# Optimization experiments

Measured on AMD Instinct MI355X. Metric: run time of the kernel, lower is better.

The kernel has to match this reference:

```python
import jax, jax.numpy as jnp
import numpy as np

NUM_HEADS = 12
HEAD_DIM = 64
HIDDEN = NUM_HEADS * HEAD_DIM


def setup_inputs() -> dict:
    key = jax.random.key(0)
    ks = jax.random.split(key, 10)
    B, S, N_ROT = 8, 1374, 1369
    s = 0.02
    return {
        "hidden_states": jax.random.normal(ks[0], (B, S, HIDDEN), jnp.float32),
        "sin": jax.random.normal(ks[1], (N_ROT, HEAD_DIM), jnp.float32),
        "cos": jax.random.normal(ks[2], (N_ROT, HEAD_DIM), jnp.float32),
        "Wq": jax.random.normal(ks[3], (HIDDEN, HIDDEN), jnp.float32) * s,
        "bq": jax.random.normal(ks[4], (HIDDEN,), jnp.float32) * s,
        "Wk": jax.random.normal(ks[5], (HIDDEN, HIDDEN), jnp.float32) * s,
        "Wv": jax.random.normal(ks[6], (HIDDEN, HIDDEN), jnp.float32) * s,
        "bv": jax.random.normal(ks[7], (HIDDEN,), jnp.float32) * s,
        "Wp": jax.random.normal(ks[8], (HIDDEN, HIDDEN), jnp.float32) * s,
        "bp": jax.random.normal(ks[9], (HIDDEN,), jnp.float32) * s,
    }


def _rotate_half(x):
    x1, x2 = jnp.split(x, 2, axis=-1)
    return jnp.concatenate([-x2, x1], axis=-1)


def _rope_apply(x, sin, cos):
    return x * cos + _rotate_half(x) * sin


def reference(hidden_states, sin, cos, Wq, bq, Wk, Wv, bv, Wp, bp):
    B, S, _ = hidden_states.shape
    scaling = HEAD_DIM ** -0.5

    def to_heads(x):  # [B,S,HIDDEN] -> [B,H,S,D]
        return x.reshape(B, S, NUM_HEADS, HEAD_DIM).transpose(0, 2, 1, 3)

    q = to_heads(hidden_states @ Wq.T + bq)
    k = to_heads(hidden_states @ Wk.T)  # no key bias (mask_k_bias)
    v = to_heads(hidden_states @ Wv.T + bv)

    # RoPE only on patch tokens (prefix = cls + register tokens untouched)
    prefix = S - sin.shape[-2]
    q = jnp.concatenate([q[:, :, :prefix], _rope_apply(q[:, :, prefix:], sin, cos)], axis=2)
    k = jnp.concatenate([k[:, :, :prefix], _rope_apply(k[:, :, prefix:], sin, cos)], axis=2)

    # eager attention: softmax in float32, no mask, no dropout (eval)
    scores = jnp.einsum("bhqd,bhkd->bhqk", q, k) * scaling
    probs = jax.nn.softmax(scores.astype(jnp.float32), axis=-1).astype(q.dtype)
    ctx = jnp.einsum("bhqk,bhkd->bqhd", probs, v).reshape(B, S, HIDDEN)
    return ctx @ Wp.T + bp
```

## Files before the change

kernel.cpp:

```cpp
#include <hip/hip_runtime.h>
#include <stdint.h>

typedef unsigned short u16;
typedef unsigned int u32;
typedef u16 u16x8 __attribute__((ext_vector_type(8)));
typedef __bf16 bf16x8 __attribute__((ext_vector_type(8)));
typedef float f32x4 __attribute__((ext_vector_type(4)));

#define S_LEN 1374
#define S_PAD 1408
#define PRE_TOK 5
#define HID 768
#define NH 12
#define MPAD 11008

__device__ __forceinline__ u16 f2bf(float f) {
    union { float f; u32 u; } v; v.f = f;
    u32 r = v.u + 0x7fffu + ((v.u >> 16) & 1u);
    return (u16)(r >> 16);
}
__device__ __forceinline__ bf16x8 as_bf(u16x8 v) { bf16x8 r; __builtin_memcpy(&r, &v, 16); return r; }
__device__ __forceinline__ bf16x8 lds_load8(const u16* p) {
    u16x8 t = *(const u16x8*)p;
    return as_bf(t);
}
__device__ __forceinline__ u32 cvtpk_bf16(float lo, float hi) {
    u32 r;
    asm("v_cvt_pk_bf16_f32 %0, %1, %2" : "=v"(r) : "v"(lo), "v"(hi));
    return r;
}
__device__ __forceinline__ float fexp2(float x) {
    float r;
    asm("v_exp_f32 %0, %1" : "=v"(r) : "v"(x));
    return r;
}
__device__ __forceinline__ void gload16(void* lds, const void* g) {
    unsigned int __attribute__((address_space(1)))* gp =
        (unsigned int __attribute__((address_space(1)))*)(unsigned long long)g;
    unsigned int __attribute__((address_space(3)))* lp =
        (unsigned int __attribute__((address_space(3)))*)(unsigned int)(unsigned long long)lds;
    __builtin_amdgcn_global_load_lds(gp, lp, 16, 0, 0);
}


__global__ __launch_bounds__(256) void pack_x(const float* __restrict__ X, u16* __restrict__ Xb) {
    size_t i = (size_t)blockIdx.x * 256 + threadIdx.x;
    size_t e = i * 8;
    const size_t TOT = (size_t)10992 * HID;
    u16x8 o = {0,0,0,0,0,0,0,0};
    if (e < TOT) {
        f32x4 a = *(const f32x4*)(X + e);
        f32x4 b = *(const f32x4*)(X + e + 4);
#pragma unroll
        for (int j = 0; j < 4; ++j) { o[j] = f2bf(a[j]); o[4 + j] = f2bf(b[j]); }
    }
    *(u16x8*)(Xb + e) = o;
}

__global__ __launch_bounds__(256) void pack_w(
    const float* __restrict__ Wq, const float* __restrict__ Wk, const float* __restrict__ Wv,
    const float* __restrict__ Wp, const float* __restrict__ bq, const float* __restrict__ bv,
    u16* __restrict__ wqkv, u16* __restrict__ wpb, float* __restrict__ bqkv)
{
    int g = blockIdx.x * 256 + threadIdx.x;
    const int QKV8 = 2304 * HID / 8;
    const int P8 = HID * HID / 8;
    if (g < QKV8) {
        int e = g * 8;
        int row = e / HID, col = e - row * HID;
        const float* src = (row < 768) ? (Wq + (size_t)row * HID + col)
                         : (row < 1536) ? (Wk + (size_t)(row - 768) * HID + col)
                                        : (Wv + (size_t)(row - 1536) * HID + col);
        u16x8 o;
#pragma unroll
        for (int j = 0; j < 8; ++j) o[j] = f2bf(src[j]);
        *(u16x8*)(wqkv + e) = o;
    } else if (g < QKV8 + P8) {
        int e = (g - QKV8) * 8;
        u16x8 o;
#pragma unroll
        for (int j = 0; j < 8; ++j) o[j] = f2bf(Wp[e + j]);
        *(u16x8*)(wpb + e) = o;
    }
    if (g < 288) {
        int e = g * 8;
#pragma unroll
        for (int j = 0; j < 8; ++j) {
            int c = e + j;
            bqkv[c] = (c < 768) ? bq[c] : (c < 1536 ? 0.f : bv[c - 1536]);
        }
    }
}


template <int EPI>
__global__ __launch_bounds__(256) void gemm_nt(
    const u16* __restrict__ A, const u16* __restrict__ B, const float* __restrict__ bias,
    float* __restrict__ Yf, u16* __restrict__ Qh, u16* __restrict__ Kh,
    u16* __restrict__ Yv, const float* __restrict__ SN, const float* __restrict__ CS,
    int N, int K)
{
    __shared__ u16 As[128 * 64];
    __shared__ u16 Bs[128 * 64];
    int tid = threadIdx.x;
    int w = tid >> 6, l = tid & 63;
    int fr = l & 15, fg = l >> 4;
    int row0 = blockIdx.y * 128;
    int col0 = blockIdx.x * 128;
    int wr = (w >> 1) * 64, wc = (w & 1) * 64;

    f32x4 zero4 = {0.f, 0.f, 0.f, 0.f};
    f32x4 acc[4][4];
#pragma unroll
    for (int m = 0; m < 4; ++m)
#pragma unroll
        for (int n = 0; n < 4; ++n) acc[m][n] = zero4;

    int srow[4], soff[4];
#pragma unroll
    for (int i = 0; i < 4; ++i) {
        int sbyte = (i * 4 + w) * 1024 + l * 16;
        int r = sbyte >> 7;
        int ir = (sbyte & 127) ^ ((r & 7) << 4);
        srow[i] = r; soff[i] = ir >> 1;
    }

    for (int kt = 0; kt < K; kt += 64) {
#pragma unroll
        for (int i = 0; i < 4; ++i) {
            int sb = (i * 4 + w) * 1024;
            gload16((char*)As + sb, A + (size_t)(row0 + srow[i]) * K + kt + soff[i]);
            gload16((char*)Bs + sb, B + (size_t)(col0 + srow[i]) * K + kt + soff[i]);
        }
        __syncthreads();
#pragma unroll
        for (int c = 0; c < 2; ++c) {
            bf16x8 af[4], bfr[4];
#pragma unroll
            for (int m = 0; m < 4; ++m) {
                int r = wr + m * 16 + fr;
                int byte_ = (c * 64 + fg * 16) ^ ((r & 7) << 4);
                af[m] = lds_load8(As + r * 64 + (byte_ >> 1));
            }
#pragma unroll
            for (int n = 0; n < 4; ++n) {
                int r = wc + n * 16 + fr;
                int byte_ = (c * 64 + fg * 16) ^ ((r & 7) << 4);
                bfr[n] = lds_load8(Bs + r * 64 + (byte_ >> 1));
            }
#pragma unroll
            for (int m = 0; m < 4; ++m)
#pragma unroll
                for (int n = 0; n < 4; ++n)
                    acc[m][n] = __builtin_amdgcn_mfma_f32_16x16x32_bf16(af[m], bfr[n], acc[m][n], 0, 0, 0);
        }
        __syncthreads();
    }

    if (EPI == 1) {
#pragma unroll
        for (int m = 0; m < 4; ++m)
#pragma unroll
            for (int n = 0; n < 4; ++n) {
                int gn = col0 + wc + n * 16 + fr;
                float bvv = bias[gn];
#pragma unroll
                for (int j = 0; j < 4; ++j) {
                    int gm = row0 + wr + m * 16 + fg * 4 + j;
                    if (gm < 10992) Yf[(size_t)gm * N + gn] = acc[m][n][j] + bvv;
                }
            }
    } else {
        int sect = col0 >= 1536 ? 2 : (col0 >= 768 ? 1 : 0);
        if (sect == 2) {
#pragma unroll
            for (int m = 0; m < 4; ++m)
#pragma unroll
                for (int n = 0; n < 4; ++n) {
                    int gn = col0 + wc + n * 16 + fr;
                    float bvv = bias[gn];
#pragma unroll
                    for (int j = 0; j < 4; ++j) {
                        int gm = row0 + wr + m * 16 + fg * 4 + j;
                        if (gm < 10992)
                            Yv[(size_t)gm * HID + (gn - 1536)] = f2bf(acc[m][n][j] + bvv);
                    }
                }
        } else {
            u16* H = sect ? Kh : Qh;
            const float QS = sect ? 1.f : 0.125f * 1.44269504088896f;
            int hh = ((col0 + wc) >> 6) - sect * NH;
            float bv4[4];
#pragma unroll
            for (int n = 0; n < 4; ++n) bv4[n] = bias[col0 + wc + n * 16 + fr];
#pragma unroll
            for (int m = 0; m < 4; ++m)
#pragma unroll
                for (int j = 0; j < 4; ++j) {
                    int gm = row0 + wr + m * 16 + fg * 4 + j;
                    if (gm < 10992) {
                        int b = gm / 1374, s = gm - b * 1374;
                        size_t ob = ((size_t)(b * NH + hh) * S_PAD + s) * 64;
#pragma unroll
                        for (int n2 = 0; n2 < 2; ++n2) {
                            int d = n2 * 16 + fr;
                            float v1 = acc[m][n2][j] + bv4[n2];
                            float v2 = acc[m][n2 + 2][j] + bv4[n2 + 2];
                            float a1 = v1, a2 = v2;
                            if (s >= PRE_TOK) {
                                size_t rr = (size_t)(s - PRE_TOK) * 64;
                                float c1 = CS[rr + d], s1 = SN[rr + d];
                                float c2 = CS[rr + d + 32], s2 = SN[rr + d + 32];
                                a1 = v1 * c1 - v2 * s1;
                                a2 = v2 * c2 + v1 * s2;
                            }
                            H[ob + d]      = f2bf(a1 * QS);
                            H[ob + d + 32] = f2bf(a2 * QS);
                        }
                    }
                }
        }
    }
}


__global__ __launch_bounds__(256) void v_pack(const u16* __restrict__ Yv, u16* __restrict__ Vt) {
    int st = blockIdx.x, bh = blockIdx.y;
    int b = bh / NH, h = bh - b * NH;
    int tid = threadIdx.x;
    int sl = tid >> 2, dg = (tid & 3) * 8;
    int s = st * 64 + sl;
    __shared__ u16 vtile[64 * 64];

    u16x8 a = {0,0,0,0,0,0,0,0}, a2 = {0,0,0,0,0,0,0,0};
    if (s < S_LEN) {
        size_t base = ((size_t)b * S_LEN + s) * HID + h * 64;
        a  = *(const u16x8*)(Yv + base + dg);
        a2 = *(const u16x8*)(Yv + base + 32 + dg);
    }
#pragma unroll
    for (int j = 0; j < 8; ++j) {
        vtile[(dg + j) * 64 + sl] = a[j];
        vtile[(32 + dg + j) * 64 + sl] = a2[j];
    }
    __syncthreads();
    int d = tid >> 2, so = (tid & 3) * 8;
    u16x8 ov0 = *(const u16x8*)(vtile + d * 64 + so);
    u16x8 ov1 = *(const u16x8*)(vtile + d * 64 + so + 32);
    size_t vrow = ((size_t)bh * 64 + d) * S_PAD + st * 64;
    *(u16x8*)(Vt + vrow + so) = ov0;
    *(u16x8*)(Vt + vrow + so + 32) = ov1;
}


#define FLASH_BODY(Kc, Vc, KsN, VsN, ktn, DO_STAGE, DO_MASK)                          \
    {                                                                                 \
        asm volatile("s_waitcnt vmcnt(0) lgkmcnt(0)" ::: "memory");                   \
        __syncthreads();                                                              \
        if (DO_STAGE) {                                                               \
            int k0n = (ktn) * 32;                                                     \
            gload16((char*)(KsN) + sb, Kb + (size_t)k0n * 64 + kfix);                 \
            gload16((char*)(VsN) + sb, Vb + (size_t)k0n + vfix);                      \
        }                                                                             \
        f32x4 sf[2];                                                                  \
        __builtin_amdgcn_s_setprio(1);                                                \
        _Pragma("unroll")                                                             \
        for (int n = 0; n < 2; ++n) {                                                 \
            f32x4 qk = zero4;                                                         \
            _Pragma("unroll")                                                         \
            for (int c = 0; c < 2; ++c) {                                             \
                int byte_ = (c * 64 + fg * 16) ^ ((fr & 7) << 4);                     \
                bf16x8 kf = lds_load8((Kc) + (n * 16 + fr) * 64 + (byte_ >> 1));      \
                qk = __builtin_amdgcn_mfma_f32_16x16x32_bf16(kf, qf[c], qk, 0, 0, 0); \
            }                                                                         \
            sf[n] = qk;                                                               \
        }                                                                             \
        __builtin_amdgcn_s_setprio(0);                                                \
        if (DO_MASK) {                                                                \
            _Pragma("unroll")                                                         \
            for (int n = 0; n < 2; ++n)                                               \
                _Pragma("unroll")                                                     \
                for (int j = 0; j < 4; ++j)                                           \
                    if (1344 + 8 * fg + 4 * n + j >= S_LEN) sf[n][j] = -1e30f;        \
        }                                                                             \
        _Pragma("unroll")                                                             \
        for (int n = 0; n < 2; ++n)                                                   \
            _Pragma("unroll")                                                         \
            for (int j = 0; j < 4; ++j) sf[n][j] = fexp2(sf[n][j]);                   \
        union PA { u32 w2[4]; bf16x8 v; } pa;                                         \
        pa.w2[0] = cvtpk_bf16(sf[0][0], sf[0][1]);                                    \
        pa.w2[1] = cvtpk_bf16(sf[0][2], sf[0][3]);                                    \
        pa.w2[2] = cvtpk_bf16(sf[1][0], sf[1][1]);                                    \
        pa.w2[3] = cvtpk_bf16(sf[1][2], sf[1][3]);                                    \
        __builtin_amdgcn_s_setprio(1);                                                \
        lsum = __builtin_amdgcn_mfma_f32_16x16x32_bf16(pa.v, ones, lsum, 0, 0, 0);    \
        _Pragma("unroll")                                                             \
        for (int nd = 0; nd < 4; ++nd) {                                              \
            int byte_ = ((nd >> 1) * 64 + fg * 16) ^ ((fr & 7) << 4);                 \
            bf16x8 vf = lds_load8((Vc) + ((nd & 1) * 16 + fr) * 64 + (byte_ >> 1));   \
            octx[nd] = __builtin_amdgcn_mfma_f32_16x16x32_bf16(pa.v, vf, octx[nd], 0, 0, 0); \
        }                                                                             \
        __builtin_amdgcn_s_setprio(0);                                                \
    }

__global__ __launch_bounds__(256, 8) void flash(
    const u16* __restrict__ Qh, const u16* __restrict__ Kh, const u16* __restrict__ Vt,
    u16* __restrict__ ctxO)
{
    int qt = blockIdx.x, bh = blockIdx.y;
    int b = bh / NH, h = bh - b * NH;
    int q0 = qt * 64;
    int tid = threadIdx.x, w = tid >> 6, l = tid & 63;
    int fr = l & 15, fg = l >> 4;

    __shared__ u16 Ks0[32 * 64], Ks1[32 * 64];
    __shared__ u16 Vs0[32 * 64], Vs1[32 * 64];

    const u16* Qb = Qh + (size_t)bh * S_PAD * 64;
    const u16* Kb = Kh + (size_t)bh * S_PAD * 64;
    const u16* Vb = Vt + (size_t)bh * 64 * S_PAD;

    bf16x8 qf[2];
    {
        int qrow = q0 + w * 16 + fr;
#pragma unroll
        for (int c = 0; c < 2; ++c)
            qf[c] = as_bf(*(const u16x8*)(Qb + (size_t)qrow * 64 + c * 32 + fg * 8));
    }

    u16x8 ones_u = {0x3F80, 0x3F80, 0x3F80, 0x3F80, 0x3F80, 0x3F80, 0x3F80, 0x3F80};
    bf16x8 ones = as_bf(ones_u);

    f32x4 zero4 = {0.f, 0.f, 0.f, 0.f};
    f32x4 octx[4] = {zero4, zero4, zero4, zero4};
    f32x4 lsum = zero4;

    int r = w * 8 + (l >> 3);
    int bb = (l & 7) * 16;
    int ir = bb ^ ((r & 7) << 4);
    int gk = ((r >> 2) & 3) * 8 + ((r >> 4) & 1) * 4 + (r & 3);
    int kfix = gk * 64 + (ir >> 1);
    int vfix = (r + (ir >> 6) * 32) * S_PAD + ((ir & 63) >> 1);
    int sb = w * 1024;

    gload16((char*)Ks0 + sb, Kb + kfix);
    gload16((char*)Vs0 + sb, Vb + vfix);

    for (int kt = 0; kt < 42; kt += 2) {
        FLASH_BODY(Ks0, Vs0, Ks1, Vs1, kt + 1, true, false);
        FLASH_BODY(Ks1, Vs1, Ks0, Vs0, kt + 2, true, false);
    }
    FLASH_BODY(Ks0, Vs0, Ks1, Vs1, 0, false, true);

#pragma unroll
    for (int j = 0; j < 4; ++j) {
        int q = q0 + w * 16 + fg * 4 + j;
        if (q < S_LEN) {
            float inv = 1.f / lsum[j];
            size_t rowb = ((size_t)b * S_LEN + q) * HID + h * 64;
#pragma unroll
            for (int nd = 0; nd < 4; ++nd)
                ctxO[rowb + nd * 16 + fr] = f2bf(octx[nd][j] * inv);
        }
    }
}


extern "C" void kernel_launch(void* const* d_in, const int* in_sizes, int n_in,
                              void* d_out, int out_size, void* d_ws, size_t ws_size,
                              hipStream_t stream) {
    (void)in_sizes; (void)n_in; (void)out_size; (void)ws_size;
    const float* X  = (const float*)d_in[0];
    const float* SN = (const float*)d_in[1];
    const float* CS = (const float*)d_in[2];
    const float* Wq = (const float*)d_in[3];
    const float* bq = (const float*)d_in[4];
    const float* Wk = (const float*)d_in[5];
    const float* Wv = (const float*)d_in[6];
    const float* bv = (const float*)d_in[7];
    const float* Wp = (const float*)d_in[8];
    const float* bp = (const float*)d_in[9];
    float* OUT = (float*)d_out;
    char* ws = (char*)d_ws;

    u16*   xb   = (u16*)(ws);
    u16*   wqkv = (u16*)(ws + 16908288);
    u16*   wpb  = (u16*)(ws + 20447232);
    float* bqkv = (float*)(ws + 21626880);
    u16*   Yv   = (u16*)(ws + 21636096);
    u16*   Qh   = (u16*)(ws + 72360960);
    u16*   Kh   = (u16*)(ws + 89662464);
    u16*   Vt   = (u16*)(ws + 106963968);
    u16*   ctx  = xb;

    pack_x<<<4128, 256, 0, stream>>>(X, xb);
    pack_w<<<1152, 256, 0, stream>>>(Wq, Wk, Wv, Wp, bq, bv, wqkv, wpb, bqkv);
    gemm_nt<2><<<dim3(18, 86), 256, 0, stream>>>(xb, wqkv, bqkv, nullptr, Qh, Kh, Yv, SN, CS, 2304, 768);
    v_pack<<<dim3(22, 96), 256, 0, stream>>>(Yv, Vt);
    flash<<<dim3(22, 96), 256, 0, stream>>>(Qh, Kh, Vt, ctx);
    gemm_nt<1><<<dim3(6, 86), 256, 0, stream>>>(ctx, wpb, bp, OUT, nullptr, nullptr, nullptr, nullptr, nullptr, 768, 768);
}
```

Before: 192.4 us.

## Double-buffer GEMM LDS tiles with K=32 steps to overlap loads with MFMA

Restructures the GEMM main loop from single-buffered 64-wide K tiles into ping-pong LDS buffers of 32-wide K tiles. The next tile's global-to-LDS load is issued before computing on the current one, which is meant to hide global memory latency behind MFMA work. LDS use stays the same, but there is now one barrier per 32-wide K step and smaller per-step MFMA batches. The swizzle also changes to 4-row XOR patterns, which may raise bank conflicts.

```diff
diff --git a/kernel.cpp b/kernel.cpp
--- a/kernel.cpp
+++ b/kernel.cpp
@@ -93,6 +93,39 @@
 }
 
 
+#define GEMM_BODY(CA, CB, NA, NB, ktn)                                                 \
+    {                                                                                  \
+        asm volatile("s_waitcnt vmcnt(0) lgkmcnt(0)" ::: "memory");                    \
+        __syncthreads();                                                               \
+        if ((ktn) < nkt) {                                                             \
+            int kk = (ktn) * 32;                                                       \
+            _Pragma("unroll")                                                          \
+            for (int i = 0; i < 2; ++i) {                                              \
+                int sb = i * 4096 + w * 1024;                                          \
+                gload16((char*)(NA) + sb, A + (size_t)(row0 + srow[i]) * K + kk + soff[i]); \
+                gload16((char*)(NB) + sb, B + (size_t)(col0 + srow[i]) * K + kk + soff[i]); \
+            }                                                                          \
+        }                                                                              \
+        bf16x8 af[4], bfr[4];                                                          \
+        _Pragma("unroll")                                                              \
+        for (int m = 0; m < 4; ++m) {                                                  \
+            int r = wr + m * 16 + fr;                                                  \
+            int byte_ = (fg * 16) ^ ((r & 3) << 4);                                    \
+            af[m] = lds_load8((CA) + r * 32 + (byte_ >> 1));                           \
+        }                                                                              \
+        _Pragma("unroll")                                                              \
+        for (int n = 0; n < 4; ++n) {                                                  \
+            int r = wc + n * 16 + fr;                                                  \
+            int byte_ = (fg * 16) ^ ((r & 3) << 4);                                    \
+            bfr[n] = lds_load8((CB) + r * 32 + (byte_ >> 1));                          \
+        }                                                                              \
+        _Pragma("unroll")                                                              \
+        for (int m = 0; m < 4; ++m)                                                    \
+            _Pragma("unroll")                                                          \
+            for (int n = 0; n < 4; ++n)                                                \
+                acc[m][n] = __builtin_amdgcn_mfma_f32_16x16x32_bf16(af[m], bfr[n], acc[m][n], 0, 0, 0); \
+    }
+
 template <int EPI>
 __global__ __launch_bounds__(256) void gemm_nt(
     const u16* __restrict__ A, const u16* __restrict__ B, const float* __restrict__ bias,
@@ -100,8 +133,8 @@
     u16* __restrict__ Yv, const float* __restrict__ SN, const float* __restrict__ CS,
     int N, int K)
 {
-    __shared__ u16 As[128 * 64];
-    __shared__ u16 Bs[128 * 64];
+    __shared__ u16 As0[128 * 32], Bs0[128 * 32];
+    __shared__ u16 As1[128 * 32], Bs1[128 * 32];
     int tid = threadIdx.x;
     int w = tid >> 6, l = tid & 63;
     int fr = l & 15, fg = l >> 4;
@@ -116,45 +149,25 @@
 #pragma unroll
         for (int n = 0; n < 4; ++n) acc[m][n] = zero4;
 
-    int srow[4], soff[4];
-#pragma unroll
-    for (int i = 0; i < 4; ++i) {
-        int sbyte = (i * 4 + w) * 1024 + l * 16;
-        int r = sbyte >> 7;
-        int ir = (sbyte & 127) ^ ((r & 7) << 4);
+    int srow[2], soff[2];
+#pragma unroll
+    for (int i = 0; i < 2; ++i) {
+        int sbyte = i * 4096 + w * 1024 + l * 16;
+        int r = sbyte >> 6;
+        int ir = (sbyte & 63) ^ ((r & 3) << 4);
         srow[i] = r; soff[i] = ir >> 1;
     }
 
-    for (int kt = 0; kt < K; kt += 64) {
-#pragma unroll
-        for (int i = 0; i < 4; ++i) {
-            int sb = (i * 4 + w) * 1024;
-            gload16((char*)As + sb, A + (size_t)(row0 + srow[i]) * K + kt + soff[i]);
-            gload16((char*)Bs + sb, B + (size_t)(col0 + srow[i]) * K + kt + soff[i]);
-        }
-        __syncthreads();
-#pragma unroll
-        for (int c = 0; c < 2; ++c) {
-            bf16x8 af[4], bfr[4];
-#pragma unroll
-            for (int m = 0; m < 4; ++m) {
-                int r = wr + m * 16 + fr;
-                int byte_ = (c * 64 + fg * 16) ^ ((r & 7) << 4);
-                af[m] = lds_load8(As + r * 64 + (byte_ >> 1));
-            }
-#pragma unroll
-            for (int n = 0; n < 4; ++n) {
-                int r = wc + n * 16 + fr;
-                int byte_ = (c * 64 + fg * 16) ^ ((r & 7) << 4);
-                bfr[n] = lds_load8(Bs + r * 64 + (byte_ >> 1));
-            }
-#pragma unroll
-            for (int m = 0; m < 4; ++m)
-#pragma unroll
-                for (int n = 0; n < 4; ++n)
-                    acc[m][n] = __builtin_amdgcn_mfma_f32_16x16x32_bf16(af[m], bfr[n], acc[m][n], 0, 0, 0);
-        }
-        __syncthreads();
+    const int nkt = K >> 5;
+#pragma unroll
+    for (int i = 0; i < 2; ++i) {
+        int sb = i * 4096 + w * 1024;
+        gload16((char*)As0 + sb, A + (size_t)(row0 + srow[i]) * K + soff[i]);
+        gload16((char*)Bs0 + sb, B + (size_t)(col0 + srow[i]) * K + soff[i]);
+    }
+    for (int kt = 0; kt < nkt; kt += 2) {
+        GEMM_BODY(As0, Bs0, As1, Bs1, kt + 1);
+        GEMM_BODY(As1, Bs1, As0, Bs0, kt + 2);
     }
 
     if (EPI == 1) {
```

After: 200.6 us. 1.04x slower.

## Load GEMM MFMA fragments directly from global memory, dropping LDS staging

Applied to the files above, without the earlier changes.

The GEMM kernel no longer stages A and B tiles through shared memory with swizzled layout and barriers. Each wave now reads its MFMA fragments straight from global memory every 32-wide K step, relying on the cache for reuse across waves, and launch bounds ask for four blocks per CU. This removes LDS traffic and syncthreads, but duplicates global and L2 loads across waves, and each lane issues strided 16-byte reads that coalesce poorly.

```diff
diff --git a/kernel.cpp b/kernel.cpp
--- a/kernel.cpp
+++ b/kernel.cpp
@@ -94,14 +94,12 @@
 
 
 template <int EPI>
-__global__ __launch_bounds__(256) void gemm_nt(
+__global__ __launch_bounds__(256, 4) void gemm_nt(
     const u16* __restrict__ A, const u16* __restrict__ B, const float* __restrict__ bias,
     float* __restrict__ Yf, u16* __restrict__ Qh, u16* __restrict__ Kh,
     u16* __restrict__ Yv, const float* __restrict__ SN, const float* __restrict__ CS,
     int N, int K)
 {
-    __shared__ u16 As[128 * 64];
-    __shared__ u16 Bs[128 * 64];
     int tid = threadIdx.x;
     int w = tid >> 6, l = tid & 63;
     int fr = l & 15, fg = l >> 4;
@@ -116,45 +114,25 @@
 #pragma unroll
         for (int n = 0; n < 4; ++n) acc[m][n] = zero4;
 
-    int srow[4], soff[4];
-#pragma unroll
-    for (int i = 0; i < 4; ++i) {
-        int sbyte = (i * 4 + w) * 1024 + l * 16;
-        int r = sbyte >> 7;
-        int ir = (sbyte & 127) ^ ((r & 7) << 4);
-        srow[i] = r; soff[i] = ir >> 1;
-    }
-
-    for (int kt = 0; kt < K; kt += 64) {
-#pragma unroll
-        for (int i = 0; i < 4; ++i) {
-            int sb = (i * 4 + w) * 1024;
-            gload16((char*)As + sb, A + (size_t)(row0 + srow[i]) * K + kt + soff[i]);
-            gload16((char*)Bs + sb, B + (size_t)(col0 + srow[i]) * K + kt + soff[i]);
-        }
-        __syncthreads();
-#pragma unroll
-        for (int c = 0; c < 2; ++c) {
-            bf16x8 af[4], bfr[4];
-#pragma unroll
-            for (int m = 0; m < 4; ++m) {
-                int r = wr + m * 16 + fr;
-                int byte_ = (c * 64 + fg * 16) ^ ((r & 7) << 4);
-                af[m] = lds_load8(As + r * 64 + (byte_ >> 1));
-            }
-#pragma unroll
-            for (int n = 0; n < 4; ++n) {
-                int r = wc + n * 16 + fr;
-                int byte_ = (c * 64 + fg * 16) ^ ((r & 7) << 4);
-                bfr[n] = lds_load8(Bs + r * 64 + (byte_ >> 1));
-            }
-#pragma unroll
-            for (int m = 0; m < 4; ++m)
-#pragma unroll
-                for (int n = 0; n < 4; ++n)
-                    acc[m][n] = __builtin_amdgcn_mfma_f32_16x16x32_bf16(af[m], bfr[n], acc[m][n], 0, 0, 0);
-        }
-        __syncthreads();
+    const u16* Ap[4];
+    const u16* Bp[4];
+#pragma unroll
+    for (int m = 0; m < 4; ++m) Ap[m] = A + (size_t)(row0 + wr + m * 16 + fr) * K + fg * 8;
+#pragma unroll
+    for (int n = 0; n < 4; ++n) Bp[n] = B + (size_t)(col0 + wc + n * 16 + fr) * K + fg * 8;
+
+#pragma unroll 2
+    for (int kt = 0; kt < K; kt += 32) {
+        bf16x8 af[4], bfr[4];
+#pragma unroll
+        for (int m = 0; m < 4; ++m) af[m] = as_bf(*(const u16x8*)(Ap[m] + kt));
+#pragma unroll
+        for (int n = 0; n < 4; ++n) bfr[n] = as_bf(*(const u16x8*)(Bp[n] + kt));
+#pragma unroll
+        for (int m = 0; m < 4; ++m)
+#pragma unroll
+            for (int n = 0; n < 4; ++n)
+                acc[m][n] = __builtin_amdgcn_mfma_f32_16x16x32_bf16(af[m], bfr[n], acc[m][n], 0, 0, 0);
     }
 
     if (EPI == 1) {
```

After: 340.1 us. +76.7%, slower.
